# Kernel tuning notes

Measured on AMD Instinct MI355X. Metric: run time of the kernel, lower is better.

## Reference

```python
import jax, jax.numpy as jnp
import numpy as np

N_POLAR = 1024
K_TARGET = 512
CRC_DEG = 11
K_POLAR = K_TARGET + CRC_DEG
BS = 65536


def _crc11_matrix(k):
    # CRC11 (5G uplink, k>19): g(x) = x^11 + x^10 + x^9 + x^5 + 1, zero-init register.
    poly = np.array([1, 1, 1, 0, 0, 0, 1, 0, 0, 0, 0, 1], dtype=np.int64)
    G = np.zeros((k, CRC_DEG), dtype=np.int64)
    for i in range(k):
        msg = np.zeros(k + CRC_DEG, dtype=np.int64)
        msg[i] = 1
        for j in range(k):
            if msg[j]:
                msg[j:j + CRC_DEG + 1] ^= poly
        G[i] = msg[k:]
    return G.astype(np.float32)


def _info_pos(n, k_polar):
    # Polarization-weight (beta-expansion) reliability design [Bioglio_Design]:
    # w(i) = sum_j b_j(i) * 2^(0.25*j); info set = k_polar most reliable indices.
    nb = int(np.log2(n))
    idx = np.arange(n)
    bits = (idx[:, None] >> np.arange(nb)[None, :]) & 1
    w = (bits * (2.0 ** (0.25 * np.arange(nb)))[None, :]).sum(axis=1)
    info = np.sort(np.argsort(w)[-k_polar:])
    return info.astype(np.int32)


def _ind_gather(n):
    # Stage-wise butterfly gather indices; pad slot n points to the zero column.
    nb = int(np.log2(n))
    g = np.full((nb, n + 1), n, dtype=np.int32)
    for s in range(nb):
        r = np.arange(n // 2)
        dest = r * 2 - np.mod(r, 2 ** s)
        g[s, dest] = dest + 2 ** s
    return g


def _subblock_idx(n):
    perm = np.array([0, 1, 2, 4, 3, 5, 6, 7, 8, 16, 9, 17, 10, 18, 11, 19,
                     12, 20, 13, 21, 14, 22, 15, 23, 24, 25, 26, 28, 27, 29, 30, 31])
    ni = np.arange(n)
    i = (32 * ni) // n
    return (perm[i] * (n // 32) + ni % (n // 32)).astype(np.int32)


def _channel_idx(n):
    # Triangular interleaver (Sec 5.4.1.3): fill rows, read columns; as index map.
    t = 0
    while t * (t + 1) // 2 < n:
        t += 1
    v = -np.ones((t, t), dtype=np.int64)
    k = 0
    for i in range(t):
        for j in range(t - i):
            if k < n:
                v[i, j] = k
            k += 1
    src = []
    for j in range(t):
        for i in range(t - j):
            if v[i, j] >= 0:
                src.append(v[i, j])
    return np.asarray(src, dtype=np.int32)


def setup_inputs() -> dict:
    key = jax.random.key(0)
    u = jax.random.randint(key, (BS, K_TARGET), 0, 2).astype(jnp.float32)
    crc_gen = jnp.asarray(_crc11_matrix(K_TARGET))
    info_pos = jnp.asarray(_info_pos(N_POLAR, K_POLAR))
    ind_gather = jnp.asarray(_ind_gather(N_POLAR))
    # E == N: rate matching is identity after sub-block interleave; fuse with
    # the uplink channel interleaver into a single output permutation.
    perm_out = jnp.asarray(_subblock_idx(N_POLAR)[_channel_idx(N_POLAR)])
    return {"u": u, "crc_gen": crc_gen, "info_pos": info_pos,
            "ind_gather": ind_gather, "perm_out": perm_out}


def reference(u, crc_gen, info_pos, ind_gather, perm_out):
    # CRC encode (GF(2)-linear => matmul mod 2), append parity.
    parity = jnp.mod(u @ crc_gen, 2.0)
    bits = jnp.concatenate([u, parity], axis=1)          # [bs, k_polar]
    bs = u.shape[0]
    n = ind_gather.shape[1] - 1
    # Subchannel allocation: scatter info+crc bits into non-frozen positions;
    # extra zero pad column at index n for the butterfly gather.
    x = jnp.zeros((bs, n + 1), u.dtype).at[:, info_pos].set(bits)
    # log2(n) butterfly stages: gather partner then XOR (mod-2 add on bits).
    for s in range(ind_gather.shape[0]):
        x = jnp.mod(x + x[:, ind_gather[s]], 2.0)
    # Sub-block interleave + rate matching (E==N) + channel interleave, fused.
    return x[:, :n][:, perm_out]
```

## Files before the change

### kernel.cpp

```cpp
#include <hip/hip_runtime.h>
#include <stdint.h>

#define NPOLAR 1024
#define KT 512
#define BLOCK 256
#define ROWS 32
#define PKP 18
#define XLP 36

__device__ __forceinline__ uint32_t fbit(float f) {
    return (__float_as_uint(f) >> 29) & 1u;
}

__global__ __launch_bounds__(BLOCK, 8) void polar_all_kernel(
    const float* __restrict__ u,
    const float* __restrict__ crc_gen,
    const int* __restrict__ info_pos,
    const int* __restrict__ perm_out,
    float* __restrict__ out)
{
    __shared__ uint32_t pk[ROWS * PKP];
    __shared__ uint32_t xl[ROWS * XLP];
    __shared__ uint32_t gc[11 * 16];
    __shared__ uint32_t mw[32];
    __shared__ uint32_t cw[32];

    const int t   = threadIdx.x;
    const int blk = blockIdx.x;
    const int r   = t >> 3;
    const int q   = t & 7;

    if (t < 32) mw[t] = 0;
    __syncthreads();

    for (int i = t; i < 523; i += BLOCK) {
        int pos = info_pos[i];
        atomicOr(&mw[pos >> 5], 1u << (pos & 31));
    }
    if (t < 176) {
        int j = t / 16, w = t % 16;
        uint32_t g = 0;
        #pragma unroll
        for (int i = 0; i < 32; ++i)
            g |= fbit(crc_gen[(32 * w + i) * 11 + j]) << i;
        gc[j * 16 + w] = g;
    }

    {
        const int slot = t & 7;
        const int w0   = (t >> 3) & 15;
        const int rpar = t >> 7;
        const float4* uv = reinterpret_cast<const float4*>(u) + (size_t)blk * (ROWS * KT / 4) + t;
        #pragma unroll
        for (int i = 0; i < 16; ++i) {
            float4 f = uv[(size_t)i * 256];
            uint32_t nib = fbit(f.x) | (fbit(f.y) << 1) | (fbit(f.z) << 2) | (fbit(f.w) << 3);
            uint32_t val = nib << (slot * 4);
            val |= __shfl_xor(val, 1);
            val |= __shfl_xor(val, 2);
            val |= __shfl_xor(val, 4);
            if (slot == 0) pk[(rpar + 2 * i) * PKP + w0] = val;
        }
    }
    __syncthreads();

    if (t < 32) {
        uint32_t c = 0;
        for (int v = 0; v < t; ++v) c += __popc(mw[v]);
        cw[t] = c;
    }

    {
        uint32_t a = pk[r * PKP + 2 * q], b = pk[r * PKP + 2 * q + 1];
        uint32_t par = 0;
        #pragma unroll
        for (int j = 0; j < 11; ++j) {
            uint32_t acc = (a & gc[j * 16 + 2 * q]) ^ (b & gc[j * 16 + 2 * q + 1]);
            par |= (uint32_t)(__popc(acc) & 1) << j;
        }
        par ^= __shfl_xor(par, 1);
        par ^= __shfl_xor(par, 2);
        par ^= __shfl_xor(par, 4);
        if (q == 0) pk[r * PKP + 16] = par;
        if (q == 1) pk[r * PKP + 17] = 0;
    }
    __syncthreads();

    uint32_t xr[4];
    {
        const uint32_t* row = &pk[r * PKP];
        #pragma unroll
        for (int j = 0; j < 4; ++j) {
            int w = 4 * q + j;
            uint32_t m = mw[w];
            uint32_t c = cw[w];
            int k = c >> 5, sh = c & 31;
            uint64_t win = (((uint64_t)row[k + 1] << 32) | row[k]) >> sh;
            uint32_t x;
            if (m == 0xFFFFFFFFu) {
                x = (uint32_t)win;
            } else {
                x = 0;
                uint32_t wv = (uint32_t)win;
                while (m) {
                    int b = __builtin_ctz(m);
                    m &= m - 1;
                    x |= (wv & 1u) << b;
                    wv >>= 1;
                }
            }
            xr[j] = x;
        }
    }

    #pragma unroll
    for (int j = 0; j < 4; ++j) {
        uint32_t v = xr[j];
        v ^= (v >> 1)  & 0x55555555u;
        v ^= (v >> 2)  & 0x33333333u;
        v ^= (v >> 4)  & 0x0F0F0F0Fu;
        v ^= (v >> 8)  & 0x00FF00FFu;
        v ^= (v >> 16) & 0x0000FFFFu;
        xr[j] = v;
    }
    xr[0] ^= xr[1]; xr[2] ^= xr[3];
    xr[0] ^= xr[2]; xr[1] ^= xr[3];
    #pragma unroll
    for (int j = 0; j < 4; ++j) {
        uint32_t p;
        p = __shfl_xor(xr[j], 1); if ((q & 1) == 0) xr[j] ^= p;
        p = __shfl_xor(xr[j], 2); if ((q & 2) == 0) xr[j] ^= p;
        p = __shfl_xor(xr[j], 4); if ((q & 4) == 0) xr[j] ^= p;
    }
    *reinterpret_cast<uint4*>(&xl[r * XLP + 4 * q]) = make_uint4(xr[0], xr[1], xr[2], xr[3]);
    __syncthreads();

    const int4 pv = reinterpret_cast<const int4*>(perm_out)[t];
    const int a0 = pv.x >> 5, s0 = pv.x & 31;
    const int a1 = pv.y >> 5, s1 = pv.y & 31;
    const int a2 = pv.z >> 5, s2 = pv.z & 31;
    const int a3 = pv.w >> 5, s3 = pv.w & 31;

    float4* outv = reinterpret_cast<float4*>(out) + (size_t)blk * (ROWS * (NPOLAR / 4)) + t;
    #pragma unroll
    for (int k = 0; k < ROWS; ++k) {
        const uint32_t* rowp = &xl[k * XLP];
        float4 o;
        o.x = (float)((rowp[a0] >> s0) & 1u);
        o.y = (float)((rowp[a1] >> s1) & 1u);
        o.z = (float)((rowp[a2] >> s2) & 1u);
        o.w = (float)((rowp[a3] >> s3) & 1u);
        outv[(size_t)k * (NPOLAR / 4)] = o;
    }
}

extern "C" void kernel_launch(void* const* d_in, const int* in_sizes, int n_in,
                              void* d_out, int out_size, void* d_ws, size_t ws_size,
                              hipStream_t stream) {
    const float* u        = (const float*)d_in[0];
    const float* crc_gen  = (const float*)d_in[1];
    const int*   info_pos = (const int*)d_in[2];
    const int*   perm_out = (const int*)d_in[4];
    float* out = (float*)d_out;

    const int rows = in_sizes[0] / KT;
    const int grid = rows / ROWS;

    polar_all_kernel<<<grid, BLOCK, 0, stream>>>(u, crc_gen, info_pos, perm_out, out);
}
```

Measured before the change: 383.6 us.

## Split fused polar kernel into pack and expand kernels via workspace

```diff
diff --git a/kernel.cpp b/kernel.cpp
--- a/kernel.cpp
+++ b/kernel.cpp
@@ -6,21 +6,19 @@
 #define BLOCK 256
 #define ROWS 32
 #define PKP 18
-#define XLP 36
+#define XLP 33
 
 __device__ __forceinline__ uint32_t fbit(float f) {
     return (__float_as_uint(f) >> 29) & 1u;
 }
 
-__global__ __launch_bounds__(BLOCK, 8) void polar_all_kernel(
+__global__ __launch_bounds__(BLOCK, 8) void polar_pack_kernel(
     const float* __restrict__ u,
     const float* __restrict__ crc_gen,
     const int* __restrict__ info_pos,
-    const int* __restrict__ perm_out,
-    float* __restrict__ out)
+    uint32_t* __restrict__ pko)
 {
     __shared__ uint32_t pk[ROWS * PKP];
-    __shared__ uint32_t xl[ROWS * XLP];
     __shared__ uint32_t gc[11 * 16];
     __shared__ uint32_t mw[32];
     __shared__ uint32_t cw[32];
@@ -132,19 +130,146 @@
         p = __shfl_xor(xr[j], 2); if ((q & 2) == 0) xr[j] ^= p;
         p = __shfl_xor(xr[j], 4); if ((q & 4) == 0) xr[j] ^= p;
     }
-    *reinterpret_cast<uint4*>(&xl[r * XLP + 4 * q]) = make_uint4(xr[0], xr[1], xr[2], xr[3]);
-    __syncthreads();
+
+    reinterpret_cast<uint4*>(pko + (size_t)blk * (ROWS * 32))[t] =
+        make_uint4(xr[0], xr[1], xr[2], xr[3]);
+}
+
+__global__ __launch_bounds__(BLOCK, 8) void polar_expand_kernel(
+    const uint32_t* __restrict__ pki,
+    const int* __restrict__ perm_out,
+    float* __restrict__ out)
+{
+    __shared__ uint32_t xl[ROWS * 32];
+    const int t   = threadIdx.x;
+    const int blk = blockIdx.x;
+
+    reinterpret_cast<uint4*>(xl)[t] =
+        reinterpret_cast<const uint4*>(pki + (size_t)blk * (ROWS * 32))[t];
 
     const int4 pv = reinterpret_cast<const int4*>(perm_out)[t];
     const int a0 = pv.x >> 5, s0 = pv.x & 31;
     const int a1 = pv.y >> 5, s1 = pv.y & 31;
     const int a2 = pv.z >> 5, s2 = pv.z & 31;
     const int a3 = pv.w >> 5, s3 = pv.w & 31;
+    __syncthreads();
 
     float4* outv = reinterpret_cast<float4*>(out) + (size_t)blk * (ROWS * (NPOLAR / 4)) + t;
     #pragma unroll
     for (int k = 0; k < ROWS; ++k) {
-        const uint32_t* rowp = &xl[k * XLP];
+        const uint32_t* rowp = &xl[k * 32];
+        float4 o;
+        o.x = (float)((rowp[a0] >> s0) & 1u);
+        o.y = (float)((rowp[a1] >> s1) & 1u);
+        o.z = (float)((rowp[a2] >> s2) & 1u);
+        o.w = (float)((rowp[a3] >> s3) & 1u);
+        outv[(size_t)k * (NPOLAR / 4)] = o;
+    }
+}
+
+__global__ __launch_bounds__(BLOCK, 8) void polar_all_kernel(
+    const float* __restrict__ u,
+    const float* __restrict__ crc_gen,
+    const int* __restrict__ info_pos,
+    const int* __restrict__ perm_out,
+    float* __restrict__ out)
+{
+    __shared__ uint32_t pk[ROWS * PKP];
+    __shared__ uint32_t xl[ROWS * 36];
+    __shared__ uint32_t gc[11 * 16];
+    __shared__ uint32_t mw[32];
+    __shared__ uint32_t cw[32];
+
+    const int t = threadIdx.x, blk = blockIdx.x, r = t >> 3, q = t & 7;
+    if (t < 32) mw[t] = 0;
+    __syncthreads();
+    for (int i = t; i < 523; i += BLOCK) {
+        int pos = info_pos[i];
+        atomicOr(&mw[pos >> 5], 1u << (pos & 31));
+    }
+    if (t < 176) {
+        int j = t / 16, w = t % 16;
+        uint32_t g = 0;
+        #pragma unroll
+        for (int i = 0; i < 32; ++i) g |= fbit(crc_gen[(32 * w + i) * 11 + j]) << i;
+        gc[j * 16 + w] = g;
+    }
+    {
+        const int slot = t & 7, w0 = (t >> 3) & 15, rpar = t >> 7;
+        const float4* uv = reinterpret_cast<const float4*>(u) + (size_t)blk * (ROWS * KT / 4) + t;
+        #pragma unroll
+        for (int i = 0; i < 16; ++i) {
+            float4 f = uv[(size_t)i * 256];
+            uint32_t nib = fbit(f.x) | (fbit(f.y) << 1) | (fbit(f.z) << 2) | (fbit(f.w) << 3);
+            uint32_t val = nib << (slot * 4);
+            val |= __shfl_xor(val, 1); val |= __shfl_xor(val, 2); val |= __shfl_xor(val, 4);
+            if (slot == 0) pk[(rpar + 2 * i) * PKP + w0] = val;
+        }
+    }
+    __syncthreads();
+    if (t < 32) {
+        uint32_t c = 0;
+        for (int v = 0; v < t; ++v) c += __popc(mw[v]);
+        cw[t] = c;
+    }
+    {
+        uint32_t a = pk[r * PKP + 2 * q], b = pk[r * PKP + 2 * q + 1];
+        uint32_t par = 0;
+        #pragma unroll
+        for (int j = 0; j < 11; ++j) {
+            uint32_t acc = (a & gc[j * 16 + 2 * q]) ^ (b & gc[j * 16 + 2 * q + 1]);
+            par |= (uint32_t)(__popc(acc) & 1) << j;
+        }
+        par ^= __shfl_xor(par, 1); par ^= __shfl_xor(par, 2); par ^= __shfl_xor(par, 4);
+        if (q == 0) pk[r * PKP + 16] = par;
+        if (q == 1) pk[r * PKP + 17] = 0;
+    }
+    __syncthreads();
+    uint32_t xr[4];
+    {
+        const uint32_t* row = &pk[r * PKP];
+        #pragma unroll
+        for (int j = 0; j < 4; ++j) {
+            int w = 4 * q + j;
+            uint32_t m = mw[w], c = cw[w];
+            int k = c >> 5, sh = c & 31;
+            uint64_t win = (((uint64_t)row[k + 1] << 32) | row[k]) >> sh;
+            uint32_t x;
+            if (m == 0xFFFFFFFFu) x = (uint32_t)win;
+            else {
+                x = 0; uint32_t wv = (uint32_t)win;
+                while (m) { int b = __builtin_ctz(m); m &= m - 1; x |= (wv & 1u) << b; wv >>= 1; }
+            }
+            xr[j] = x;
+        }
+    }
+    #pragma unroll
+    for (int j = 0; j < 4; ++j) {
+        uint32_t v = xr[j];
+        v ^= (v >> 1) & 0x55555555u; v ^= (v >> 2) & 0x33333333u;
+        v ^= (v >> 4) & 0x0F0F0F0Fu; v ^= (v >> 8) & 0x00FF00FFu;
+        v ^= (v >> 16) & 0x0000FFFFu;
+        xr[j] = v;
+    }
+    xr[0] ^= xr[1]; xr[2] ^= xr[3]; xr[0] ^= xr[2]; xr[1] ^= xr[3];
+    #pragma unroll
+    for (int j = 0; j < 4; ++j) {
+        uint32_t p;
+        p = __shfl_xor(xr[j], 1); if ((q & 1) == 0) xr[j] ^= p;
+        p = __shfl_xor(xr[j], 2); if ((q & 2) == 0) xr[j] ^= p;
+        p = __shfl_xor(xr[j], 4); if ((q & 4) == 0) xr[j] ^= p;
+    }
+    *reinterpret_cast<uint4*>(&xl[r * 36 + 4 * q]) = make_uint4(xr[0], xr[1], xr[2], xr[3]);
+    __syncthreads();
+    const int4 pv = reinterpret_cast<const int4*>(perm_out)[t];
+    const int a0 = pv.x >> 5, s0 = pv.x & 31;
+    const int a1 = pv.y >> 5, s1 = pv.y & 31;
+    const int a2 = pv.z >> 5, s2 = pv.z & 31;
+    const int a3 = pv.w >> 5, s3 = pv.w & 31;
+    float4* outv = reinterpret_cast<float4*>(out) + (size_t)blk * (ROWS * (NPOLAR / 4)) + t;
+    #pragma unroll
+    for (int k = 0; k < ROWS; ++k) {
+        const uint32_t* rowp = &xl[k * 36];
         float4 o;
         o.x = (float)((rowp[a0] >> s0) & 1u);
         o.y = (float)((rowp[a1] >> s1) & 1u);
@@ -164,7 +289,13 @@
     float* out = (float*)d_out;
 
     const int rows = in_sizes[0] / KT;
-    const int grid = rows / ROWS;
-
-    polar_all_kernel<<<grid, BLOCK, 0, stream>>>(u, crc_gen, info_pos, perm_out, out);
-}
+    const size_t need = (size_t)rows * 32 * sizeof(uint32_t);
+
+    if (ws_size >= need) {
+        uint32_t* pk = (uint32_t*)d_ws;
+        polar_pack_kernel<<<rows / ROWS, BLOCK, 0, stream>>>(u, crc_gen, info_pos, pk);
+        polar_expand_kernel<<<rows / ROWS, BLOCK, 0, stream>>>(pk, perm_out, out);
+    } else {
+        polar_all_kernel<<<rows / ROWS, BLOCK, 0, stream>>>(u, crc_gen, info_pos, perm_out, out);
+    }
+}
```

New measurement: 387.7 us. Within noise of the previous version (+1.1%).
